# Performance work log

Measured on AMD Instinct MI355X. Metric: run time of the kernel, lower is better.

The kernel has to match this reference:

```python
import jax, jax.numpy as jnp
import numpy as np

B, N, S, C, NS = 2, 20000, 1024, 256, 16
RADIUS, HMIN, HMAX = 0.05, -0.02, 0.04
NA, ND = 12, 4
EPS = 1e-5  # BatchNorm eps


def setup_inputs() -> dict:
    key = jax.random.key(0)
    ks = jax.random.split(key, 40)
    def rn(k, shape, scale=0.05):
        return jax.random.normal(k, shape, jnp.float32) * scale
    inp = {
        "xyz": jax.random.uniform(ks[0], (B, N, 3), jnp.float32),
        "new_xyz": jax.random.uniform(ks[1], (B, S, 3), jnp.float32),
        "view_rot": jax.random.normal(ks[2], (B, S, 3, 3), jnp.float32),
        "features": jax.random.normal(ks[3], (B, C, N), jnp.float32),
    }
    i = 4
    for li, (o, ci) in enumerate([(512, C + 3), (256, 512), (256, 256)], 1):
        inp[f"mlp{li}_w"] = rn(ks[i], (o, ci)); inp[f"mlp{li}_b"] = rn(ks[i + 1], (o,))
        inp[f"mlp{li}_g"] = jnp.ones((o,), jnp.float32) + rn(ks[i + 2], (o,), 0.01)
        inp[f"mlp{li}_be"] = rn(ks[i + 3], (o,)); i += 4
    for name in ("c1", "c2"):
        inp[f"{name}_w"] = rn(ks[i], (256, 256)); inp[f"{name}_b"] = rn(ks[i + 1], (256,))
        inp[f"{name}_g"] = jnp.ones((256,), jnp.float32) + rn(ks[i + 2], (256,), 0.01)
        inp[f"{name}_be"] = rn(ks[i + 3], (256,)); i += 4
    inp["c3_w"] = rn(ks[i], (NA * ND * 2, 256)); inp["c3_b"] = rn(ks[i + 1], (NA * ND * 2,))
    return inp


def _bn(x, g, be):  # eval-mode BatchNorm with running_mean=0, running_var=1
    return x * (g / jnp.sqrt(1.0 + EPS)) + be


def _forward(xyz, new_xyz, view_rot, features,
             mlp1_w, mlp1_b, mlp1_g, mlp1_be,
             mlp2_w, mlp2_b, mlp2_g, mlp2_be,
             mlp3_w, mlp3_b, mlp3_g, mlp3_be,
             c1_w, c1_b, c1_g, c1_be,
             c2_w, c2_b, c2_g, c2_be,
             c3_w, c3_b):
    # ---- cylinder query (CUDA kernel math: r = rot @ (p - c), cylinder axis = x) ----
    # computed per rotation row to keep intermediates at (B,S,N) each
    comp = []
    for i in range(3):
        rw = view_rot[:, :, i, :]  # (B,S,3)
        comp.append(jnp.einsum('bsj,bpj->bsp', rw, xyz) - jnp.sum(rw * new_xyz, -1)[..., None])
    xr, yr, zr = comp  # each (B,S,N)
    mask = (yr * yr + zr * zr < RADIUS * RADIUS) & (xr > HMIN) & (xr < HMAX)
    # first-NS valid indices per seed (ascending), pad with first valid (0 if none)
    vals = jnp.where(mask, jnp.arange(N, dtype=jnp.int32), N)  # (B,S,N)
    neg_top, _ = jax.lax.top_k(-vals, NS)
    idx = -neg_top  # (B,S,NS) ascending
    first = idx[..., :1]
    first = jnp.where(first >= N, 0, first)
    idx = jnp.where(idx >= N, first, idx)
    # ---- group ----
    b_ix = jnp.arange(B)[:, None, None]
    g_xyz = xyz[b_ix, idx]                                  # (B,S,NS,3)
    g_feat = jnp.transpose(features, (0, 2, 1))[b_ix, idx]  # (B,S,NS,C)
    diff = (g_xyz - new_xyz[:, :, None, :]) / RADIUS        # normalize_xyz
    rot_xyz = jnp.einsum('bsnk,bskj->bsnj', diff, view_rot)  # rotate_xyz: diff @ rot
    h = jnp.concatenate([rot_xyz, g_feat], axis=-1)          # (B,S,NS,C+3)
    # ---- SharedMLP (1x1 conv2d + BN + ReLU) ----
    for w, bb, g, be in ((mlp1_w, mlp1_b, mlp1_g, mlp1_be),
                         (mlp2_w, mlp2_b, mlp2_g, mlp2_be),
                         (mlp3_w, mlp3_b, mlp3_g, mlp3_be)):
        h = jax.nn.relu(_bn(jnp.einsum('bsnc,oc->bsno', h, w) + bb, g, be))
    h = h.max(axis=2)  # max-pool over samples -> (B,S,256)
    # ---- pointwise conv1d head ----
    h = jax.nn.relu(_bn(jnp.einsum('bsc,oc->bso', h, c1_w) + c1_b, c1_g, c1_be))
    h = jax.nn.relu(_bn(jnp.einsum('bsc,oc->bso', h, c2_w) + c2_b, c2_g, c2_be))
    out = jnp.einsum('bsc,oc->bso', h, c3_w) + c3_b  # (B,S,NA*ND*2)
    return out


def reference(xyz, new_xyz, view_rot, features,
              mlp1_w, mlp1_b, mlp1_g, mlp1_be,
              mlp2_w, mlp2_b, mlp2_g, mlp2_be,
              mlp3_w, mlp3_b, mlp3_g, mlp3_be,
              c1_w, c1_b, c1_g, c1_be,
              c2_w, c2_b, c2_g, c2_be,
              c3_w, c3_b):
    return _forward(xyz, new_xyz, view_rot, features,
                    mlp1_w, mlp1_b, mlp1_g, mlp1_be,
                    mlp2_w, mlp2_b, mlp2_g, mlp2_be,
                    mlp3_w, mlp3_b, mlp3_g, mlp3_be,
                    c1_w, c1_b, c1_g, c1_be,
                    c2_w, c2_b, c2_g, c2_be,
                    c3_w, c3_b)
```

## Files before the change

kernel.cpp:

```cpp
#include <hip/hip_runtime.h>
#include <hip/hip_bf16.h>
#include <stdint.h>
#include <limits.h>

#define B_   2
#define N_   20000
#define S_   1024
#define C_   256
#define NS_  16
#define NQ   (B_ * S_)
#define M_   (NQ * NS_)
#define K1P  288
#define O1   512
#define O2   256
#define O3   256
#define OUTC 96

#define R2C   ((float)(0.05 * 0.05))
#define HMINC ((float)(-0.02))
#define HMAXC ((float)(0.04))

#define GDIM   16
#define GCELLS (GDIM * GDIM * GDIM)
#define GTOT   (B_ * GCELLS)
#define CAP    256

__device__ __forceinline__ unsigned short f2b(float f) {
    union { float f; unsigned int i; } x; x.f = f;
    unsigned int r = x.i + 0x7FFFu + ((x.i >> 16) & 1u);
    return (unsigned short)(r >> 16);
}

__device__ __forceinline__ void gl16(const unsigned short* g, unsigned short* l) {
    __builtin_amdgcn_global_load_lds(
        (const __attribute__((address_space(1))) unsigned int*)g,
        (__attribute__((address_space(3))) unsigned int*)l,
        16, 0, 0);
}

__global__ __launch_bounds__(256) void prep_w123z(const float* __restrict__ m1w,
                                                  const float* __restrict__ m2w,
                                                  const float* __restrict__ m3w,
                                                  unsigned short* __restrict__ w1p,
                                                  unsigned short* __restrict__ w2p,
                                                  unsigned short* __restrict__ w3p,
                                                  int* __restrict__ gcnt) {
    int i = blockIdx.x * 256 + threadIdx.x;
    if (i < GTOT) gcnt[i] = 0;
    if (i < O1 * K1P) {
        int o = i / K1P, k = i - o * K1P;
        float v = 0.0f;
        if (k < 256)      v = m1w[o * 259 + 3 + k];
        else if (k < 259) v = m1w[o * 259 + (k - 256)];
        w1p[i] = (k < 259) ? f2b(v) : (unsigned short)0;
    } else if (i < O1 * K1P + O2 * 512) {
        int j = i - O1 * K1P;
        w2p[j] = f2b(m2w[j]);
    } else if (i < O1 * K1P + O2 * 512 + O3 * 256) {
        int j = i - O1 * K1P - O2 * 512;
        w3p[j] = f2b(m3w[j]);
    }
}

__global__ __launch_bounds__(256) void transpose_feat(const float* __restrict__ feat,
                                                      unsigned short* __restrict__ feat_t) {
    __shared__ float tile[32][33];
    int n0 = blockIdx.x * 32, c0 = blockIdx.y * 32, b = blockIdx.z;
    int t = threadIdx.x;
    int nl = t & 31;
#pragma unroll
    for (int i = 0; i < 4; ++i) {
        int cl = (t >> 5) + i * 8;
        tile[cl][nl] = feat[((size_t)(b * C_ + c0 + cl)) * N_ + n0 + nl];
    }
    __syncthreads();
    int nr = t >> 3, c4 = (t & 7) * 4;
    ushort4 v;
    v.x = f2b(tile[c4 + 0][nr]);
    v.y = f2b(tile[c4 + 1][nr]);
    v.z = f2b(tile[c4 + 2][nr]);
    v.w = f2b(tile[c4 + 3][nr]);
    *(ushort4*)(feat_t + ((size_t)(b * N_ + n0 + nr)) * C_ + c0 + c4) = v;
}

__device__ __forceinline__ int cell_of(float px, float py, float pz, int b) {
    int cx = (int)(px * (float)GDIM); cx = min(GDIM - 1, max(0, cx));
    int cy = (int)(py * (float)GDIM); cy = min(GDIM - 1, max(0, cy));
    int cz = (int)(pz * (float)GDIM); cz = min(GDIM - 1, max(0, cz));
    return b * GCELLS + cz * (GDIM * GDIM) + cy * GDIM + cx;
}

__global__ __launch_bounds__(256) void grid_count(const float* __restrict__ xyz,
                                                  int* __restrict__ counts) {
    int i = blockIdx.x * 256 + threadIdx.x;
    if (i < B_ * N_) {
        int b = i / N_;
        const float* p = xyz + (size_t)i * 3;
        atomicAdd(counts + cell_of(p[0], p[1], p[2], b), 1);
    }
}

__global__ __launch_bounds__(256) void grid_scan(const int* __restrict__ counts,
                                                 int* __restrict__ start,
                                                 int* __restrict__ cursor) {
    __shared__ int part[256];
    int t = threadIdx.x;
    int local[32];
    int s = 0;
#pragma unroll
    for (int i = 0; i < 32; ++i) { local[i] = counts[t * 32 + i]; s += local[i]; }
    part[t] = s;
    __syncthreads();
    if (t == 0) {
        int r = 0;
        for (int i = 0; i < 256; ++i) { int x = part[i]; part[i] = r; r += x; }
    }
    __syncthreads();
    int r = part[t];
#pragma unroll
    for (int i = 0; i < 32; ++i) {
        start[t * 32 + i] = r;
        cursor[t * 32 + i] = r;
        r += local[i];
    }
    if (t == 255) start[GTOT] = r;
}

__global__ __launch_bounds__(256) void grid_scatter(const float* __restrict__ xyz,
                                                    int* __restrict__ cursor,
                                                    float4* __restrict__ sorted) {
    int i = blockIdx.x * 256 + threadIdx.x;
    if (i < B_ * N_) {
        int b = i / N_, n = i - b * N_;
        const float* p = xyz + (size_t)i * 3;
        float px = p[0], py = p[1], pz = p[2];
        int pos = atomicAdd(cursor + cell_of(px, py, pz, b), 1);
        sorted[pos] = make_float4(px, py, pz, __int_as_float(n));
    }
}

__device__ __forceinline__ void sort16(int* buf, int cnt, int lane) {
    asm volatile("s_waitcnt lgkmcnt(0)" ::: "memory");
    __builtin_amdgcn_sched_barrier(0);
    int a0 = INT_MAX, a1 = INT_MAX, a2 = INT_MAX, a3 = INT_MAX;
    if (lane < cnt)       a0 = buf[lane];
    if (lane + 64 < cnt)  a1 = buf[lane + 64];
    if (lane + 128 < cnt) a2 = buf[lane + 128];
    if (lane + 192 < cnt) a3 = buf[lane + 192];
#pragma unroll
    for (int t = 0; t < NS_; ++t) {
        int v = a0, sl = 0;
        if (a1 < v) { v = a1; sl = 1; }
        if (a2 < v) { v = a2; sl = 2; }
        if (a3 < v) { v = a3; sl = 3; }
        int pp = (sl << 6) | lane;
#pragma unroll
        for (int off = 1; off < 64; off <<= 1) {
            int ov = __shfl_xor(v, off);
            int op = __shfl_xor(pp, off);
            if (ov < v) { v = ov; pp = op; }
        }
        if ((pp & 63) == lane) {
            int s = pp >> 6;
            if (s == 0) a0 = INT_MAX;
            else if (s == 1) a1 = INT_MAX;
            else if (s == 2) a2 = INT_MAX;
            else a3 = INT_MAX;
        }
        if (lane == 0) buf[t] = v;
    }
    asm volatile("s_waitcnt lgkmcnt(0)" ::: "memory");
    __builtin_amdgcn_sched_barrier(0);
}

__global__ __launch_bounds__(256) void cyl_query_grid(const float* __restrict__ new_xyz,
                                                      const float* __restrict__ view_rot,
                                                      const float4* __restrict__ sorted,
                                                      const int* __restrict__ cell_start,
                                                      int* __restrict__ idx_out) {
#pragma clang fp contract(off)
    int w = threadIdx.x >> 6, lane = threadIdx.x & 63;
    int q = blockIdx.x;
    int b = q >> 10;

    __shared__ int bufs[4][CAP];
    __shared__ int tots[4];
    __shared__ int spnE[4][64];
    __shared__ int spnS[4][64];
    int* buf = bufs[w];

    const float* nq = new_xyz + (size_t)q * 3;
    float qx = nq[0], qy = nq[1], qz = nq[2];
    const float* rp = view_rot + (size_t)q * 9;
    float R[9];
#pragma unroll
    for (int i = 0; i < 9; ++i) R[i] = rp[i];
    float dq0 = (R[0]*qx + R[1]*qy) + R[2]*qz;
    float dq1 = (R[3]*qx + R[4]*qy) + R[5]*qz;
    float dq2 = (R[6]*qx + R[7]*qy) + R[8]*qz;

    int x0 = 0, x1 = GDIM - 1, y0 = 0, y1 = GDIM - 1, z0 = 0, z1 = GDIM - 1;
    {
        float det = R[0]*(R[4]*R[8]-R[5]*R[7])
                  - R[1]*(R[3]*R[8]-R[5]*R[6])
                  + R[2]*(R[3]*R[7]-R[4]*R[6]);
        float adet = fabsf(det);
        if (adet > 1e-30f) {
            float id = 1.0f / det;
            float m00 = (R[4]*R[8]-R[5]*R[7])*id, m01 = (R[2]*R[7]-R[1]*R[8])*id, m02 = (R[1]*R[5]-R[2]*R[4])*id;
            float m10 = (R[5]*R[6]-R[3]*R[8])*id, m11 = (R[0]*R[8]-R[2]*R[6])*id, m12 = (R[2]*R[3]-R[0]*R[5])*id;
            float m20 = (R[3]*R[7]-R[4]*R[6])*id, m21 = (R[1]*R[6]-R[0]*R[7])*id, m22 = (R[0]*R[4]-R[1]*R[3])*id;
            const float mid = 0.5f * (HMINC + HMAXC);
            const float hh  = 0.5f * (HMAXC - HMINC);
            float cx = qx + m00 * mid, cy = qy + m10 * mid, cz = qz + m20 * mid;
            float ex = hh * fabsf(m00) + 0.05f * sqrtf(m01*m01 + m02*m02);
            float ey = hh * fabsf(m10) + 0.05f * sqrtf(m11*m11 + m12*m12);
            float ez = hh * fabsf(m20) + 0.05f * sqrtf(m21*m21 + m22*m22);
            ex = ex * 1.002f + 1e-3f;
            ey = ey * 1.002f + 1e-3f;
            ez = ez * 1.002f + 1e-3f;
            x0 = (int)fmaxf(0.0f, fminf((float)(GDIM - 1), floorf((cx - ex) * (float)GDIM)));
            x1 = (int)fmaxf(0.0f, fminf((float)(GDIM - 1), floorf((cx + ex) * (float)GDIM)));
            y0 = (int)fmaxf(0.0f, fminf((float)(GDIM - 1), floorf((cy - ey) * (float)GDIM)));
            y1 = (int)fmaxf(0.0f, fminf((float)(GDIM - 1), floorf((cy + ey) * (float)GDIM)));
            z0 = (int)fmaxf(0.0f, fminf((float)(GDIM - 1), floorf((cz - ez) * (float)GDIM)));
            z1 = (int)fmaxf(0.0f, fminf((float)(GDIM - 1), floorf((cz + ez) * (float)GDIM)));
        }
    }

    int ny = y1 - y0 + 1, nz = z1 - z0 + 1;
    int cnt = 0, tot = 0;
    int cbase = b * GCELLS;

    {
        int NR = ny * nz;
        int nr_w = (NR - w + 3) >> 2;
        const float inv16 = 0.0625f, half = 0.03125f;
        float ax = (fabsf(R[0]) + fabsf(R[1]) + fabsf(R[2])) * half + 2e-4f;
        float ay = (fabsf(R[3]) + fabsf(R[4]) + fabsf(R[5])) * half + 2e-4f;
        float az = (fabsf(R[6]) + fabsf(R[7]) + fabsf(R[8])) * half + 2e-4f;
        int sl = 0, el = 0;
        if (lane < nr_w) {
            int ri = w + (lane << 2);
            int zi = ri / ny;
            int yi = ri - zi * ny;
            float cy0 = (y0 + yi + 0.5f) * inv16;
            float cz0 = (z0 + zi + 0.5f) * inv16;
            float cx0 = (x0 + 0.5f) * inv16;
            float xr = (R[0]*cx0 + R[1]*cy0) + R[2]*cz0 - dq0;
            float yr = (R[3]*cx0 + R[4]*cy0) + R[5]*cz0 - dq1;
            float zr = (R[6]*cx0 + R[7]*cy0) + R[8]*cz0 - dq2;
            float sx = R[0] * inv16, sy = R[3] * inv16, sz = R[6] * inv16;
            int xa = 1 << 28, xb = -1;
            for (int cx = x0; cx <= x1; ++cx) {
                bool px = (xr + ax > HMINC) && (xr - ax < HMAXC);
                float dy = fmaxf(fabsf(yr) - ay, 0.0f);
                float dz = fmaxf(fabsf(zr) - az, 0.0f);
                bool pr = (dy*dy + dz*dz) < (R2C + 1e-5f);
                if (px && pr) { if (cx < xa) xa = cx; xb = cx; }
                xr += sx; yr += sy; zr += sz;
            }
            if (xb >= xa) {
                int cid = cbase + (z0 + zi) * (GDIM * GDIM) + (y0 + yi) * GDIM;
                sl = cell_start[cid + xa];
                el = cell_start[cid + xb + 1];
            }
        }

        int len = el - sl;
        int incl = len;
#pragma unroll
        for (int off = 1; off < 64; off <<= 1) {
            int v = __shfl_up(incl, off);
            if (lane >= off) incl += v;
        }
        int T = __shfl(incl, 63);
        spnE[w][lane] = incl - len;
        spnS[w][lane] = sl;
        asm volatile("s_waitcnt lgkmcnt(0)" ::: "memory");
        __builtin_amdgcn_sched_barrier(0);

        for (int g0 = 0; g0 < T; g0 += 64) {
            int g = g0 + lane;
            bool m = false; int n = 0;
            if (g < T) {
                int lo = 0, hi = 63;
#pragma unroll
                for (int it = 0; it < 6; ++it) {
                    int mid = (lo + hi + 1) >> 1;
                    if (spnE[w][mid] <= g) lo = mid; else hi = mid - 1;
                }
                int p = spnS[w][lo] + (g - spnE[w][lo]);
                float4 v = sorted[p];
                n = __float_as_int(v.w);
                float px = v.x, py = v.y, pz = v.z;
                float xr = ((R[0]*px + R[1]*py) + R[2]*pz) - dq0;
                float yr = ((R[3]*px + R[4]*py) + R[5]*pz) - dq1;
                float zr = ((R[6]*px + R[7]*py) + R[8]*pz) - dq2;
                m = ((yr*yr + zr*zr) < R2C) && (xr > HMINC) && (xr < HMAXC);
            }
            unsigned long long bal = __ballot(m);
            if (m) {
                int pos = cnt + __popcll(bal & ((1ull << lane) - 1ull));
                buf[pos] = n;
            }
            int h = __popcll(bal);
            cnt += h; tot += h;
            if (cnt > CAP - 64) { sort16(buf, cnt, lane); cnt = NS_; }
        }
    }

    sort16(buf, cnt, lane);
    if (lane == 0) tots[w] = tot;
    __syncthreads();

    if (w == 0) {
        int cand = bufs[lane >> 4][lane & 15];
        int myv = INT_MAX;
#pragma unroll
        for (int t = 0; t < NS_; ++t) {
            int v = cand, pp = lane;
#pragma unroll
            for (int off = 1; off < 64; off <<= 1) {
                int ov = __shfl_xor(v, off);
                int op = __shfl_xor(pp, off);
                if (ov < v) { v = ov; pp = op; }
            }
            if (lane == t) myv = v;
            if (pp == lane) cand = INT_MAX;
        }
        int tt = tots[0] + tots[1] + tots[2] + tots[3];
        int total = tt < NS_ ? tt : NS_;
        int first = (tt > 0) ? __shfl(myv, 0) : 0;
        if (lane < NS_)
            idx_out[q * NS_ + lane] = (lane < total) ? myv : first;
    }
}

__global__ __launch_bounds__(256) void build_h0(const float* __restrict__ xyz,
                                                const float* __restrict__ new_xyz,
                                                const float* __restrict__ view_rot,
                                                const unsigned short* __restrict__ feat_t,
                                                const int* __restrict__ idxs,
                                                unsigned short* __restrict__ h0) {
#pragma clang fp contract(off)
    int q = blockIdx.x;
    int b = q >> 10;
    int t = threadIdx.x;
    __shared__ int pidx[NS_];
    if (t < NS_) pidx[t] = idxs[q * NS_ + t];
    __syncthreads();

#pragma unroll
    for (int pass = 0; pass < 2; ++pass) {
        int n = pass * 8 + (t >> 5);
        int p = pidx[n];
        uint4 v = *(const uint4*)(feat_t + ((size_t)(b * N_ + p)) * C_ + (t & 31) * 8);
        *(uint4*)(h0 + (size_t)(q * NS_ + n) * K1P + (t & 31) * 8) = v;
    }

    if (t < NS_) {
        int n = t, p = pidx[n];
        const float* pp = xyz + ((size_t)b * N_ + p) * 3;
        const float* nq = new_xyz + (size_t)q * 3;
        float dx = (pp[0] - nq[0]) / 0.05f;
        float dy = (pp[1] - nq[1]) / 0.05f;
        float dz = (pp[2] - nq[2]) / 0.05f;
        const float* rp = view_rot + (size_t)q * 9;
        float r0 = (dx * rp[0] + dy * rp[3]) + dz * rp[6];
        float r1 = (dx * rp[1] + dy * rp[4]) + dz * rp[7];
        float r2 = (dx * rp[2] + dy * rp[5]) + dz * rp[8];
        size_t row = (size_t)(q * NS_ + n) * K1P;
        h0[row + 256] = f2b(r0);
        h0[row + 257] = f2b(r1);
        h0[row + 258] = f2b(r2);
    }
    for (int e = t; e < NS_ * 29; e += 256) {
        int n = e / 29, c = 259 + (e - n * 29);
        h0[(size_t)(q * NS_ + n) * K1P + c] = 0;
    }
}

typedef float f32x4 __attribute__((ext_vector_type(4)));
typedef short s16x8 __attribute__((ext_vector_type(8)));

__global__ __launch_bounds__(256) void gemm_bn_relu(const unsigned short* __restrict__ A,
                                                    const unsigned short* __restrict__ W,
                                                    const float* __restrict__ bias,
                                                    const float* __restrict__ gam,
                                                    const float* __restrict__ bet,
                                                    unsigned short* __restrict__ out,
                                                    int M, int Nn, int K) {
    __shared__ __align__(16) unsigned short As[128 * 32];
    __shared__ __align__(16) unsigned short Bs[128 * 32];
    int tid  = threadIdx.x;
    int lane = tid & 63, wave = tid >> 6;
    int m0 = blockIdx.x * 128, n0 = blockIdx.y * 128;
    int wm = (wave >> 1) * 64, wn = (wave & 1) * 64;

    f32x4 acc[4][4] = {};

    for (int k0 = 0; k0 < K; k0 += 32) {
        __syncthreads();
#pragma unroll
        for (int j = 0; j < 2; ++j) {
            int e = j * 256 + tid;
            int r = e >> 2, c8 = (e & 3) << 3;
            gl16(A + (size_t)(m0 + r) * K + k0 + c8, &As[e * 8]);
            gl16(W + (size_t)(n0 + r) * K + k0 + c8, &Bs[e * 8]);
        }
        __syncthreads();

        int kq = (lane >> 4) * 8, rr = lane & 15;
        s16x8 af[4], bfr[4];
#pragma unroll
        for (int i = 0; i < 4; ++i) af[i]  = *(const s16x8*)&As[(wm + i * 16 + rr) * 32 + kq];
#pragma unroll
        for (int j = 0; j < 4; ++j) bfr[j] = *(const s16x8*)&Bs[(wn + j * 16 + rr) * 32 + kq];
#pragma unroll
        for (int i = 0; i < 4; ++i)
#pragma unroll
            for (int j = 0; j < 4; ++j)
                acc[i][j] = __builtin_amdgcn_mfma_f32_16x16x32_bf16(af[i], bfr[j], acc[i][j], 0, 0, 0);
    }

    float inv = 1.0f / sqrtf(1.0f + 1e-5f);
    int col = lane & 15, rq = (lane >> 4) * 4;
#pragma unroll
    for (int j = 0; j < 4; ++j) {
        int n = n0 + wn + j * 16 + col;
        float sc = gam[n] * inv;
        float tb = bias[n] * sc + bet[n];
#pragma unroll
        for (int i = 0; i < 4; ++i) {
            int mbase = m0 + wm + i * 16 + rq;
#pragma unroll
            for (int r = 0; r < 4; ++r) {
                float v = acc[i][j][r] * sc + tb;
                v = fmaxf(v, 0.0f);
                out[(size_t)(mbase + r) * Nn + n] = f2b(v);
            }
        }
    }
}

__global__ __launch_bounds__(512) void gemm23_pool(const unsigned short* __restrict__ A,
                                                   const unsigned short* __restrict__ W2,
                                                   const float* __restrict__ bias2,
                                                   const float* __restrict__ gam2,
                                                   const float* __restrict__ bet2,
                                                   const unsigned short* __restrict__ W3,
                                                   const float* __restrict__ bias3,
                                                   const float* __restrict__ gam3,
                                                   const float* __restrict__ bet3,
                                                   const float* __restrict__ c1w,
                                                   const float* __restrict__ c2w,
                                                   const float* __restrict__ c3w,
                                                   unsigned short* __restrict__ wprep,
                                                   unsigned short* __restrict__ hp) {
    __shared__ __align__(16) unsigned short As[128 * 32];
    __shared__ __align__(16) unsigned short Bs[256 * 32];
    __shared__ __align__(16) unsigned short H2[128 * 256];
    int tid = threadIdx.x, lane = tid & 63, wave = tid >> 6;
    int m0 = blockIdx.x * 128;
    int wm = (wave >> 1) * 32, wn = (wave & 1) * 128;
    int kq = (lane >> 4) * 8, rr = lane & 15;
    int col = lane & 15, rq = (lane >> 4) * 4;
    float inv = 1.0f / sqrtf(1.0f + 1e-5f);

    f32x4 acc[2][8] = {};

    for (int k0 = 0; k0 < 512; k0 += 32) {
        __syncthreads();
        {
            int r = tid >> 2, c8 = (tid & 3) << 3;
            gl16(A + (size_t)(m0 + r) * 512 + k0 + c8, &As[tid * 8]);
        }
#pragma unroll
        for (int j = 0; j < 2; ++j) {
            int e = j * 512 + tid;
            int r = e >> 2, c8 = (e & 3) << 3;
            gl16(W2 + (size_t)r * 512 + k0 + c8, &Bs[e * 8]);
        }
        __syncthreads();
        s16x8 af[2], bf[8];
#pragma unroll
        for (int i = 0; i < 2; ++i) af[i] = *(const s16x8*)&As[(wm + i * 16 + rr) * 32 + kq];
#pragma unroll
        for (int j = 0; j < 8; ++j) bf[j] = *(const s16x8*)&Bs[(wn + j * 16 + rr) * 32 + kq];
#pragma unroll
        for (int i = 0; i < 2; ++i)
#pragma unroll
            for (int j = 0; j < 8; ++j)
                acc[i][j] = __builtin_amdgcn_mfma_f32_16x16x32_bf16(af[i], bf[j], acc[i][j], 0, 0, 0);
    }

    {
        int e0 = blockIdx.x * 768;
        for (int e = e0 + tid; e < e0 + 768; e += 512) {
            int l = e >> 16, j = e & 65535, row = j >> 8, kcol = j & 255;
            float v;
            if (l == 0)      v = c1w[j];
            else if (l == 1) v = c2w[j];
            else             v = (row < OUTC) ? c3w[row * 256 + kcol] : 0.0f;
            int c = kcol & 127;
            wprep[l * 65536 + (kcol >> 7) * 32768 + row * 128 + (c ^ ((row & 7) << 3))] = f2b(v);
        }
    }

#pragma unroll
    for (int j = 0; j < 8; ++j) {
        int n = wn + j * 16 + col;
        float sc = gam2[n] * inv;
        float tb = bias2[n] * sc + bet2[n];
#pragma unroll
        for (int i = 0; i < 2; ++i) {
#pragma unroll
            for (int r = 0; r < 4; ++r) {
                int row = wm + i * 16 + rq + r;
                float v = fmaxf(acc[i][j][r] * sc + tb, 0.0f);
                *(unsigned short*)((char*)H2 + row * 512 + ((2 * n) ^ ((row & 7) << 4))) = f2b(v);
            }
        }
    }

#pragma unroll
    for (int i = 0; i < 2; ++i)
#pragma unroll
        for (int j = 0; j < 8; ++j) acc[i][j] = (f32x4){0.f, 0.f, 0.f, 0.f};

    for (int k0 = 0; k0 < 256; k0 += 32) {
        __syncthreads();
#pragma unroll
        for (int j = 0; j < 2; ++j) {
            int e = j * 512 + tid;
            int r = e >> 2, c8 = (e & 3) << 3;
            gl16(W3 + (size_t)r * 256 + k0 + c8, &Bs[e * 8]);
        }
        __syncthreads();
        s16x8 af[2], bf[8];
#pragma unroll
        for (int i = 0; i < 2; ++i) {
            int row = wm + i * 16 + rr;
            af[i] = *(const s16x8*)((const char*)H2 + row * 512 + ((2 * (k0 + kq)) ^ ((row & 7) << 4)));
        }
#pragma unroll
        for (int j = 0; j < 8; ++j) bf[j] = *(const s16x8*)&Bs[(wn + j * 16 + rr) * 32 + kq];
#pragma unroll
        for (int i = 0; i < 2; ++i)
#pragma unroll
            for (int j = 0; j < 8; ++j)
                acc[i][j] = __builtin_amdgcn_mfma_f32_16x16x32_bf16(af[i], bf[j], acc[i][j], 0, 0, 0);
    }

    int qbase = (m0 + wm) >> 4;
#pragma unroll
    for (int j = 0; j < 8; ++j) {
        int n = wn + j * 16 + col;
        float sc = gam3[n] * inv;
        float tb = bias3[n] * sc + bet3[n];
#pragma unroll
        for (int i = 0; i < 2; ++i) {
            float mx = 0.0f;
#pragma unroll
            for (int r = 0; r < 4; ++r)
                mx = fmaxf(mx, acc[i][j][r] * sc + tb);
            mx = fmaxf(mx, __shfl_xor(mx, 16, 64));
            mx = fmaxf(mx, __shfl_xor(mx, 32, 64));
            if (lane < 16)
                hp[(size_t)(qbase + i) * 256 + n] = f2b(mx);
        }
    }
}

__device__ __forceinline__ void head_gemm(const unsigned short* __restrict__ act,
                                          unsigned short* __restrict__ Ws,
                                          const unsigned short* __restrict__ Wp,
                                          int tid, int lane, int wn, f32x4 acc[4][4]) {
    int kq = (lane >> 4) * 8, rr = lane & 15;
    for (int h = 0; h < 2; ++h) {
        __syncthreads();
        const unsigned short* src = Wp + h * 32768;
#pragma unroll
        for (int p = 0; p < 16; ++p)
            gl16(src + (p * 256 + tid) * 8, Ws + (p * 256 + tid) * 8);
        __syncthreads();
        int k0 = h * 128;
#pragma unroll
        for (int kk = 0; kk < 128; kk += 32) {
            s16x8 af[4], bf[4];
#pragma unroll
            for (int i = 0; i < 4; ++i) {
                int row = i * 16 + rr;
                af[i] = *(const s16x8*)((const char*)act + row * 512 + ((2 * (k0 + kk + kq)) ^ ((row & 7) << 4)));
            }
#pragma unroll
            for (int j = 0; j < 4; ++j) {
                int row = wn + j * 16 + rr;
                bf[j] = *(const s16x8*)&Ws[row * 128 + ((kk + kq) ^ ((row & 7) << 3))];
            }
#pragma unroll
            for (int i = 0; i < 4; ++i)
#pragma unroll
                for (int j = 0; j < 4; ++j)
                    acc[i][j] = __builtin_amdgcn_mfma_f32_16x16x32_bf16(af[i], bf[j], acc[i][j], 0, 0, 0);
        }
    }
}

__global__ __launch_bounds__(256) void head_fused(const unsigned short* __restrict__ hp,
                                                  const unsigned short* __restrict__ wp,
                                                  const float* __restrict__ c1b,
                                                  const float* __restrict__ c1g, const float* __restrict__ c1be,
                                                  const float* __restrict__ c2b,
                                                  const float* __restrict__ c2g, const float* __restrict__ c2be,
                                                  const float* __restrict__ c3b,
                                                  float* __restrict__ out) {
    __shared__ __align__(16) unsigned short actA[64 * 256];
    __shared__ __align__(16) unsigned short actB[64 * 256];
    __shared__ __align__(16) unsigned short Ws[256 * 128];
    int tid = threadIdx.x, lane = tid & 63, wave = tid >> 6;
    int q0 = blockIdx.x * 64;
    int wn = wave * 64, col = lane & 15, rq = (lane >> 4) * 4;
    float inv = 1.0f / sqrtf(1.0f + 1e-5f);

#pragma unroll
    for (int j = 0; j < 8; ++j) {
        int c = j * 256 + tid;
        int row = c >> 5, cb = c & 31;
        uint4 v = *(const uint4*)(hp + (size_t)(q0 + row) * 256 + cb * 8);
        *(uint4*)((char*)actA + row * 512 + (((unsigned)cb << 4) ^ ((row & 7) << 4))) = v;
    }

    f32x4 acc[4][4];

#pragma unroll
    for (int i = 0; i < 4; ++i)
#pragma unroll
        for (int j = 0; j < 4; ++j) acc[i][j] = (f32x4){0.f, 0.f, 0.f, 0.f};
    head_gemm(actA, Ws, wp, tid, lane, wn, acc);
#pragma unroll
    for (int j = 0; j < 4; ++j) {
        int n = wn + j * 16 + col;
        float sc = c1g[n] * inv, tb = c1b[n] * sc + c1be[n];
#pragma unroll
        for (int i = 0; i < 4; ++i)
#pragma unroll
            for (int r = 0; r < 4; ++r) {
                int row = i * 16 + rq + r;
                float v = fmaxf(acc[i][j][r] * sc + tb, 0.0f);
                *(unsigned short*)((char*)actB + row * 512 + ((2 * n) ^ ((row & 7) << 4))) = f2b(v);
            }
    }

#pragma unroll
    for (int i = 0; i < 4; ++i)
#pragma unroll
        for (int j = 0; j < 4; ++j) acc[i][j] = (f32x4){0.f, 0.f, 0.f, 0.f};
    head_gemm(actB, Ws, wp + 65536, tid, lane, wn, acc);
#pragma unroll
    for (int j = 0; j < 4; ++j) {
        int n = wn + j * 16 + col;
        float sc = c2g[n] * inv, tb = c2b[n] * sc + c2be[n];
#pragma unroll
        for (int i = 0; i < 4; ++i)
#pragma unroll
            for (int r = 0; r < 4; ++r) {
                int row = i * 16 + rq + r;
                float v = fmaxf(acc[i][j][r] * sc + tb, 0.0f);
                *(unsigned short*)((char*)actA + row * 512 + ((2 * n) ^ ((row & 7) << 4))) = f2b(v);
            }
    }

#pragma unroll
    for (int i = 0; i < 4; ++i)
#pragma unroll
        for (int j = 0; j < 4; ++j) acc[i][j] = (f32x4){0.f, 0.f, 0.f, 0.f};
    head_gemm(actA, Ws, wp + 131072, tid, lane, wn, acc);
#pragma unroll
    for (int j = 0; j < 4; ++j) {
        int n = wn + j * 16 + col;
        if (n < OUTC) {
            float bb = c3b[n];
#pragma unroll
            for (int i = 0; i < 4; ++i)
#pragma unroll
                for (int r = 0; r < 4; ++r)
                    out[(size_t)(q0 + i * 16 + rq + r) * OUTC + n] = acc[i][j][r] + bb;
        }
    }
}

extern "C" void kernel_launch(void* const* d_in, const int* in_sizes, int n_in,
                              void* d_out, int out_size, void* d_ws, size_t ws_size,
                              hipStream_t stream) {
    const float* xyz      = (const float*)d_in[0];
    const float* new_xyz  = (const float*)d_in[1];
    const float* view_rot = (const float*)d_in[2];
    const float* feat     = (const float*)d_in[3];
    const float* m1w = (const float*)d_in[4];
    const float* m1b = (const float*)d_in[5];
    const float* m1g = (const float*)d_in[6];
    const float* m1be= (const float*)d_in[7];
    const float* m2w = (const float*)d_in[8];
    const float* m2b = (const float*)d_in[9];
    const float* m2g = (const float*)d_in[10];
    const float* m2be= (const float*)d_in[11];
    const float* m3w = (const float*)d_in[12];
    const float* m3b = (const float*)d_in[13];
    const float* m3g = (const float*)d_in[14];
    const float* m3be= (const float*)d_in[15];
    const float* c1w = (const float*)d_in[16];
    const float* c1b = (const float*)d_in[17];
    const float* c1g = (const float*)d_in[18];
    const float* c1be= (const float*)d_in[19];
    const float* c2w = (const float*)d_in[20];
    const float* c2b = (const float*)d_in[21];
    const float* c2g = (const float*)d_in[22];
    const float* c2be= (const float*)d_in[23];
    const float* c3w = (const float*)d_in[24];
    const float* c3b = (const float*)d_in[25];

    char* ws = (char*)d_ws;
    int*            idxs = (int*)ws;
    unsigned short* w1p  = (unsigned short*)(ws + 131072);
    unsigned short* w2p  = (unsigned short*)(ws + 425984);
    unsigned short* w3p  = (unsigned short*)(ws + 688128);
    unsigned short* h0   = (unsigned short*)(ws + 819200);
    unsigned short* hp   = (unsigned short*)(ws + 819200);
    unsigned short* wprep= (unsigned short*)(ws + 1867776);
    char*           h1b  = ws + 19693568;
    unsigned short* h1   = (unsigned short*)h1b;
    unsigned short* featt= (unsigned short*)(h1b + 12582912);
    float4*         srt  = (float4*)(h1b + 0);
    int*            gcnt = (int*)(h1b + 640000);
    int*            gsta = (int*)(h1b + 672768);
    int*            gcur = (int*)(h1b + 705552);

    hipLaunchKernelGGL(prep_w123z, dim3((O1 * K1P + O2 * 512 + O3 * 256) / 256), dim3(256), 0, stream,
                       m1w, m2w, m3w, w1p, w2p, w3p, gcnt);
    hipLaunchKernelGGL(grid_count, dim3((B_ * N_ + 255) / 256), dim3(256), 0, stream, xyz, gcnt);
    hipLaunchKernelGGL(grid_scan, dim3(1), dim3(256), 0, stream, gcnt, gsta, gcur);
    hipLaunchKernelGGL(grid_scatter, dim3((B_ * N_ + 255) / 256), dim3(256), 0, stream, xyz, gcur, srt);
    hipLaunchKernelGGL(cyl_query_grid, dim3(NQ), dim3(256), 0, stream,
                       new_xyz, view_rot, srt, gsta, idxs);
    hipLaunchKernelGGL(transpose_feat, dim3(N_ / 32, C_ / 32, B_), dim3(256), 0, stream, feat, featt);
    hipLaunchKernelGGL(build_h0, dim3(NQ), dim3(256), 0, stream, xyz, new_xyz, view_rot, featt, idxs, h0);
    hipLaunchKernelGGL(gemm_bn_relu, dim3(M_ / 128, O1 / 128), dim3(256), 0, stream,
                       h0, w1p, m1b, m1g, m1be, h1, M_, O1, K1P);
    hipLaunchKernelGGL(gemm23_pool, dim3(M_ / 128), dim3(512), 0, stream,
                       h1, w2p, m2b, m2g, m2be, w3p, m3b, m3g, m3be,
                       c1w, c2w, c3w, wprep, hp);
    hipLaunchKernelGGL(head_fused, dim3(NQ / 64), dim3(256), 0, stream,
                       hp, wprep, c1b, c1g, c1be, c2b, c2g, c2be, c3b, (float*)d_out);
}
```

Measured before the change: 249.3 us.

## Fuse feature transpose into query kernel, shrink gemm23 tile, wave-scan grid

The feature transpose becomes extra blocks of the cylinder query kernel, so both run in one launch and can overlap. The grid prefix scan replaces a serial single-thread loop with wave shuffle scans. gemm23_pool now takes 64 rows per block instead of 128, which doubles the block count and cuts LDS use, at the cost of reloading W2 and W3 tiles twice as often per row. The c1/c2/c3 weight prep per block is re-split to match the new grid.

```diff
diff --git a/kernel.cpp b/kernel.cpp
--- a/kernel.cpp
+++ b/kernel.cpp
@@ -24,6 +24,7 @@
 #define GCELLS (GDIM * GDIM * GDIM)
 #define GTOT   (B_ * GCELLS)
 #define CAP    256
+#define TBLK   10000
 
 __device__ __forceinline__ unsigned short f2b(float f) {
     union { float f; unsigned int i; } x; x.f = f;
@@ -62,27 +63,6 @@
     }
 }
 
-__global__ __launch_bounds__(256) void transpose_feat(const float* __restrict__ feat,
-                                                      unsigned short* __restrict__ feat_t) {
-    __shared__ float tile[32][33];
-    int n0 = blockIdx.x * 32, c0 = blockIdx.y * 32, b = blockIdx.z;
-    int t = threadIdx.x;
-    int nl = t & 31;
-#pragma unroll
-    for (int i = 0; i < 4; ++i) {
-        int cl = (t >> 5) + i * 8;
-        tile[cl][nl] = feat[((size_t)(b * C_ + c0 + cl)) * N_ + n0 + nl];
-    }
-    __syncthreads();
-    int nr = t >> 3, c4 = (t & 7) * 4;
-    ushort4 v;
-    v.x = f2b(tile[c4 + 0][nr]);
-    v.y = f2b(tile[c4 + 1][nr]);
-    v.z = f2b(tile[c4 + 2][nr]);
-    v.w = f2b(tile[c4 + 3][nr]);
-    *(ushort4*)(feat_t + ((size_t)(b * N_ + n0 + nr)) * C_ + c0 + c4) = v;
-}
-
 __device__ __forceinline__ int cell_of(float px, float py, float pz, int b) {
     int cx = (int)(px * (float)GDIM); cx = min(GDIM - 1, max(0, cx));
     int cy = (int)(py * (float)GDIM); cy = min(GDIM - 1, max(0, cy));
@@ -103,20 +83,23 @@
 __global__ __launch_bounds__(256) void grid_scan(const int* __restrict__ counts,
                                                  int* __restrict__ start,
                                                  int* __restrict__ cursor) {
-    __shared__ int part[256];
-    int t = threadIdx.x;
+    __shared__ int wsum[4];
+    int t = threadIdx.x, lane = t & 63, wv = t >> 6;
     int local[32];
     int s = 0;
 #pragma unroll
     for (int i = 0; i < 32; ++i) { local[i] = counts[t * 32 + i]; s += local[i]; }
-    part[t] = s;
+    int incl = s;
+#pragma unroll
+    for (int off = 1; off < 64; off <<= 1) {
+        int u = __shfl_up(incl, off);
+        if (lane >= off) incl += u;
+    }
+    if (lane == 63) wsum[wv] = incl;
     __syncthreads();
-    if (t == 0) {
-        int r = 0;
-        for (int i = 0; i < 256; ++i) { int x = part[i]; part[i] = r; r += x; }
-    }
-    __syncthreads();
-    int r = part[t];
+    int add = 0;
+    for (int i = 0; i < wv; ++i) add += wsum[i];
+    int r = incl - s + add;
 #pragma unroll
     for (int i = 0; i < 32; ++i) {
         start[t * 32 + i] = r;
@@ -173,20 +156,47 @@
     __builtin_amdgcn_sched_barrier(0);
 }
 
-__global__ __launch_bounds__(256) void cyl_query_grid(const float* __restrict__ new_xyz,
-                                                      const float* __restrict__ view_rot,
-                                                      const float4* __restrict__ sorted,
-                                                      const int* __restrict__ cell_start,
-                                                      int* __restrict__ idx_out) {
+__global__ __launch_bounds__(256) void query_transpose(const float* __restrict__ new_xyz,
+                                                       const float* __restrict__ view_rot,
+                                                       const float4* __restrict__ sorted,
+                                                       const int* __restrict__ cell_start,
+                                                       const float* __restrict__ feat,
+                                                       int* __restrict__ idx_out,
+                                                       unsigned short* __restrict__ feat_t) {
 #pragma clang fp contract(off)
-    int w = threadIdx.x >> 6, lane = threadIdx.x & 63;
-    int q = blockIdx.x;
-    int b = q >> 10;
-
     __shared__ int bufs[4][CAP];
     __shared__ int tots[4];
     __shared__ int spnE[4][64];
     __shared__ int spnS[4][64];
+    __shared__ float tile[32][33];
+
+    if (blockIdx.x >= NQ) {
+        int t5 = blockIdx.x - NQ;
+        int n0 = (t5 % 625) * 32;
+        int rem = t5 / 625;
+        int c0 = (rem & 7) * 32;
+        int b = rem >> 3;
+        int t = threadIdx.x;
+        int nl = t & 31;
+#pragma unroll
+        for (int i = 0; i < 4; ++i) {
+            int cl = (t >> 5) + i * 8;
+            tile[cl][nl] = feat[((size_t)(b * C_ + c0 + cl)) * N_ + n0 + nl];
+        }
+        __syncthreads();
+        int nr = t >> 3, c4 = (t & 7) * 4;
+        ushort4 v;
+        v.x = f2b(tile[c4 + 0][nr]);
+        v.y = f2b(tile[c4 + 1][nr]);
+        v.z = f2b(tile[c4 + 2][nr]);
+        v.w = f2b(tile[c4 + 3][nr]);
+        *(ushort4*)(feat_t + ((size_t)(b * N_ + n0 + nr)) * C_ + c0 + c4) = v;
+        return;
+    }
+
+    int w = threadIdx.x >> 6, lane = threadIdx.x & 63;
+    int q = blockIdx.x;
+    int b = q >> 10;
     int* buf = bufs[w];
 
     const float* nq = new_xyz + (size_t)q * 3;
@@ -458,21 +468,21 @@
                                                    const float* __restrict__ c3w,
                                                    unsigned short* __restrict__ wprep,
                                                    unsigned short* __restrict__ hp) {
-    __shared__ __align__(16) unsigned short As[128 * 32];
+    __shared__ __align__(16) unsigned short As[64 * 32];
     __shared__ __align__(16) unsigned short Bs[256 * 32];
-    __shared__ __align__(16) unsigned short H2[128 * 256];
+    __shared__ __align__(16) unsigned short H2[64 * 256];
     int tid = threadIdx.x, lane = tid & 63, wave = tid >> 6;
-    int m0 = blockIdx.x * 128;
-    int wm = (wave >> 1) * 32, wn = (wave & 1) * 128;
+    int m0 = blockIdx.x * 64;
+    int wm = (wave >> 1) * 16, wn = (wave & 1) * 128;
     int kq = (lane >> 4) * 8, rr = lane & 15;
     int col = lane & 15, rq = (lane >> 4) * 4;
     float inv = 1.0f / sqrtf(1.0f + 1e-5f);
 
-    f32x4 acc[2][8] = {};
+    f32x4 acc[8] = {};
 
     for (int k0 = 0; k0 < 512; k0 += 32) {
         __syncthreads();
-        {
+        if (tid < 256) {
             int r = tid >> 2, c8 = (tid & 3) << 3;
             gl16(A + (size_t)(m0 + r) * 512 + k0 + c8, &As[tid * 8]);
         }
@@ -483,21 +493,18 @@
             gl16(W2 + (size_t)r * 512 + k0 + c8, &Bs[e * 8]);
         }
         __syncthreads();
-        s16x8 af[2], bf[8];
-#pragma unroll
-        for (int i = 0; i < 2; ++i) af[i] = *(const s16x8*)&As[(wm + i * 16 + rr) * 32 + kq];
+        s16x8 af = *(const s16x8*)&As[(wm + rr) * 32 + kq];
+        s16x8 bf[8];
 #pragma unroll
         for (int j = 0; j < 8; ++j) bf[j] = *(const s16x8*)&Bs[(wn + j * 16 + rr) * 32 + kq];
 #pragma unroll
-        for (int i = 0; i < 2; ++i)
-#pragma unroll
-            for (int j = 0; j < 8; ++j)
-                acc[i][j] = __builtin_amdgcn_mfma_f32_16x16x32_bf16(af[i], bf[j], acc[i][j], 0, 0, 0);
+        for (int j = 0; j < 8; ++j)
+            acc[j] = __builtin_amdgcn_mfma_f32_16x16x32_bf16(af, bf[j], acc[j], 0, 0, 0);
     }
 
     {
-        int e0 = blockIdx.x * 768;
-        for (int e = e0 + tid; e < e0 + 768; e += 512) {
+        int e = blockIdx.x * 384 + tid;
+        if (tid < 384) {
             int l = e >> 16, j = e & 65535, row = j >> 8, kcol = j & 255;
             float v;
             if (l == 0)      v = c1w[j];
@@ -514,20 +521,15 @@
         float sc = gam2[n] * inv;
         float tb = bias2[n] * sc + bet2[n];
 #pragma unroll
-        for (int i = 0; i < 2; ++i) {
-#pragma unroll
-            for (int r = 0; r < 4; ++r) {
-                int row = wm + i * 16 + rq + r;
-                float v = fmaxf(acc[i][j][r] * sc + tb, 0.0f);
-                *(unsigned short*)((char*)H2 + row * 512 + ((2 * n) ^ ((row & 7) << 4))) = f2b(v);
-            }
-        }
-    }
-
-#pragma unroll
-    for (int i = 0; i < 2; ++i)
-#pragma unroll
-        for (int j = 0; j < 8; ++j) acc[i][j] = (f32x4){0.f, 0.f, 0.f, 0.f};
+        for (int r = 0; r < 4; ++r) {
+            int row = wm + rq + r;
+            float v = fmaxf(acc[j][r] * sc + tb, 0.0f);
+            *(unsigned short*)((char*)H2 + row * 512 + ((2 * n) ^ ((row & 7) << 4))) = f2b(v);
+        }
+    }
+
+#pragma unroll
+    for (int j = 0; j < 8; ++j) acc[j] = (f32x4){0.f, 0.f, 0.f, 0.f};
 
     for (int k0 = 0; k0 < 256; k0 += 32) {
         __syncthreads();
@@ -538,19 +540,14 @@
             gl16(W3 + (size_t)r * 256 + k0 + c8, &Bs[e * 8]);
         }
         __syncthreads();
-        s16x8 af[2], bf[8];
-#pragma unroll
-        for (int i = 0; i < 2; ++i) {
-            int row = wm + i * 16 + rr;
-            af[i] = *(const s16x8*)((const char*)H2 + row * 512 + ((2 * (k0 + kq)) ^ ((row & 7) << 4)));
-        }
+        int row = wm + rr;
+        s16x8 af = *(const s16x8*)((const char*)H2 + row * 512 + ((2 * (k0 + kq)) ^ ((row & 7) << 4)));
+        s16x8 bf[8];
 #pragma unroll
         for (int j = 0; j < 8; ++j) bf[j] = *(const s16x8*)&Bs[(wn + j * 16 + rr) * 32 + kq];
 #pragma unroll
-        for (int i = 0; i < 2; ++i)
-#pragma unroll
-            for (int j = 0; j < 8; ++j)
-                acc[i][j] = __builtin_amdgcn_mfma_f32_16x16x32_bf16(af[i], bf[j], acc[i][j], 0, 0, 0);
+        for (int j = 0; j < 8; ++j)
+            acc[j] = __builtin_amdgcn_mfma_f32_16x16x32_bf16(af, bf[j], acc[j], 0, 0, 0);
     }
 
     int qbase = (m0 + wm) >> 4;
@@ -559,17 +556,14 @@
         int n = wn + j * 16 + col;
         float sc = gam3[n] * inv;
         float tb = bias3[n] * sc + bet3[n];
-#pragma unroll
-        for (int i = 0; i < 2; ++i) {
-            float mx = 0.0f;
-#pragma unroll
-            for (int r = 0; r < 4; ++r)
-                mx = fmaxf(mx, acc[i][j][r] * sc + tb);
-            mx = fmaxf(mx, __shfl_xor(mx, 16, 64));
-            mx = fmaxf(mx, __shfl_xor(mx, 32, 64));
-            if (lane < 16)
-                hp[(size_t)(qbase + i) * 256 + n] = f2b(mx);
-        }
+        float mx = 0.0f;
+#pragma unroll
+        for (int r = 0; r < 4; ++r)
+            mx = fmaxf(mx, acc[j][r] * sc + tb);
+        mx = fmaxf(mx, __shfl_xor(mx, 16, 64));
+        mx = fmaxf(mx, __shfl_xor(mx, 32, 64));
+        if (lane < 16)
+            hp[(size_t)qbase * 256 + n] = f2b(mx);
     }
 }
 
@@ -742,13 +736,12 @@
     hipLaunchKernelGGL(grid_count, dim3((B_ * N_ + 255) / 256), dim3(256), 0, stream, xyz, gcnt);
     hipLaunchKernelGGL(grid_scan, dim3(1), dim3(256), 0, stream, gcnt, gsta, gcur);
     hipLaunchKernelGGL(grid_scatter, dim3((B_ * N_ + 255) / 256), dim3(256), 0, stream, xyz, gcur, srt);
-    hipLaunchKernelGGL(cyl_query_grid, dim3(NQ), dim3(256), 0, stream,
-                       new_xyz, view_rot, srt, gsta, idxs);
-    hipLaunchKernelGGL(transpose_feat, dim3(N_ / 32, C_ / 32, B_), dim3(256), 0, stream, feat, featt);
+    hipLaunchKernelGGL(query_transpose, dim3(NQ + TBLK), dim3(256), 0, stream,
+                       new_xyz, view_rot, srt, gsta, feat, idxs, featt);
     hipLaunchKernelGGL(build_h0, dim3(NQ), dim3(256), 0, stream, xyz, new_xyz, view_rot, featt, idxs, h0);
     hipLaunchKernelGGL(gemm_bn_relu, dim3(M_ / 128, O1 / 128), dim3(256), 0, stream,
                        h0, w1p, m1b, m1g, m1be, h1, M_, O1, K1P);
-    hipLaunchKernelGGL(gemm23_pool, dim3(M_ / 128), dim3(512), 0, stream,
+    hipLaunchKernelGGL(gemm23_pool, dim3(M_ / 64), dim3(512), 0, stream,
                        h1, w2p, m2b, m2g, m2be, w3p, m3b, m3g, m3be,
                        c1w, c2w, c3w, wprep, hp);
     hipLaunchKernelGGL(head_fused, dim3(NQ / 64), dim3(256), 0, stream,
```

Result: faster. 239.0 us (median of 2 runs) (-4.1%).
